# Kernel optimization log

Hardware: AMD Instinct MI355X
Metric: run time of the kernel (lower is better)

Reference implementation:

```python
import jax, jax.numpy as jnp
import numpy as np

B, D, E, K = 8192, 1024, 8, 2048  # tokens, dim, num_experts, k (per-expert capacity)


def setup_inputs() -> dict:
    key = jax.random.key(0)
    ks = jax.random.split(key, 5)
    x = jax.random.normal(ks[0], (B, D), dtype=jnp.float32)
    Wr = jax.random.normal(ks[1], (D, E), dtype=jnp.float32) * 0.02
    br = jnp.zeros((E,), jnp.float32)
    W1 = jax.random.normal(ks[2], (E, D, 4 * D), dtype=jnp.float32) * 0.02
    b1 = jnp.zeros((E, 4 * D), jnp.float32)
    W2 = jax.random.normal(ks[3], (E, 4 * D, D), dtype=jnp.float32) * 0.02
    b2 = jnp.zeros((E, D), jnp.float32)
    return {"x": x, "Wr": Wr, "br": br, "W1": W1, "b1": b1, "W2": W2, "b2": b2}


def _dispatch_weights(x, Wr, br):
    # Expert-choice routing: softmax over experts per token, each expert picks top-K tokens.
    gate = jax.nn.softmax(x @ Wr + br, axis=-1)          # [B, E]
    vals, idx = jax.lax.top_k(gate.T, K)                 # [E, K] each
    w = jnp.zeros((x.shape[0], E), x.dtype)
    w = w.at[idx.reshape(-1), jnp.repeat(jnp.arange(E), K)].set(vals.reshape(-1))
    # torch source builds dispatch_weights via .tolist(), detaching it from autograd
    return jax.lax.stop_gradient(w)                      # [B, E]


def reference(x, Wr, br, W1, b1, W2, b2):
    w = _dispatch_weights(x, Wr, br)                     # [B, E]
    mask = (w > 0).astype(x.dtype)                       # [B, E]
    xm = x[None, :, :] * mask.T[:, :, None]              # [E, B, D] (dense masked input, as in source)
    h = jax.nn.relu(jnp.einsum('ebd,edh->ebh', xm, W1) + b1[:, None, :])   # [E, B, 4D]
    y = jnp.einsum('ebh,ehd->ebd', h, W2) + b2[:, None, :]                 # [E, B, D]
    out = jnp.einsum('ebd,be->bd', y, w)                 # weighted combine over experts
    return out
```

## Files before the change

### kernel.cpp

```cpp
#include <hip/hip_runtime.h>
#include <hip/hip_bf16.h>

#define BTOK 8192
#define DDIM 1024
#define NEXP 8
#define KCAP 2048
#define HDIM 4096
#define MB ((size_t)1048576)

typedef __attribute__((ext_vector_type(4))) float f32x4;
typedef __attribute__((ext_vector_type(8))) short bf16x8;

__device__ __forceinline__ unsigned short f2bf(float f) {
    union { float f; unsigned u; } v; v.f = f;
    unsigned r = v.u + 0x7fffu + ((v.u >> 16) & 1u);
    return (unsigned short)(r >> 16);
}
__device__ __forceinline__ float bf2f(unsigned short u) {
    union { unsigned u; float f; } v; v.u = ((unsigned)u) << 16;
    return v.f;
}

typedef __attribute__((address_space(3))) unsigned int lds_u32;
typedef __attribute__((address_space(1))) const unsigned int glb_u32;
__device__ __forceinline__ void gl_lds16(const void* g, void* l) {
    __builtin_amdgcn_global_load_lds((glb_u32*)g, (lds_u32*)l, 16, 0, 0);
}

__global__ __launch_bounds__(256) void prep_kernel(
    const float* __restrict__ x, const float* __restrict__ Wr,
    const float* __restrict__ br, const float* __restrict__ W1,
    const float* __restrict__ W2, float* __restrict__ gateT,
    unsigned short* __restrict__ xb, unsigned short* __restrict__ w1t,
    unsigned short* __restrict__ w2t, int* __restrict__ inv) {
    __shared__ char smem[NEXP * DDIM * 4];
    int bid = blockIdx.x;
    int t = threadIdx.x;
    if (bid < BTOK / 4) {
        float (*wr_s)[DDIM] = (float (*)[DDIM])smem;
        for (int i = t; i < NEXP * DDIM; i += 256) {
            int e = i >> 10, d = i & 1023;
            wr_s[e][d] = Wr[d * NEXP + e];
        }
        if (t < 32) inv[(size_t)(t >> 2) * BTOK + bid * 4 + (t & 3)] = -1;
        __syncthreads();
        int wid = t >> 6, lane = t & 63;
        int b = bid * 4 + wid;
        const float4* xr = (const float4*)(x + (size_t)b * DDIM);
        float4 xv[4];
#pragma unroll
        for (int j = 0; j < 4; j++) xv[j] = xr[j * 64 + lane];
#pragma unroll
        for (int j = 0; j < 4; j++) {
            short4 s;
            s.x = (short)f2bf(xv[j].x); s.y = (short)f2bf(xv[j].y);
            s.z = (short)f2bf(xv[j].z); s.w = (short)f2bf(xv[j].w);
            *(short4*)(xb + (size_t)b * DDIM + (j * 64 + lane) * 4) = s;
        }
        double acc[NEXP];
#pragma unroll
        for (int e = 0; e < NEXP; e++) {
            double a = 0.0;
#pragma unroll
            for (int j = 0; j < 4; j++) {
                float4 wv = ((const float4*)&wr_s[e][0])[j * 64 + lane];
                a += (double)xv[j].x * wv.x + (double)xv[j].y * wv.y
                   + (double)xv[j].z * wv.z + (double)xv[j].w * wv.w;
            }
#pragma unroll
            for (int s = 1; s < 64; s <<= 1) a += __shfl_xor(a, s, 64);
            acc[e] = a + (double)br[e];
        }
        if (lane == 0) {
            double mx = acc[0];
#pragma unroll
            for (int e = 1; e < NEXP; e++) mx = fmax(mx, acc[e]);
            double p[NEXP]; double ssum = 0.0;
#pragma unroll
            for (int e = 0; e < NEXP; e++) { p[e] = exp(acc[e] - mx); ssum += p[e]; }
            double is = 1.0 / ssum;
#pragma unroll
            for (int e = 0; e < NEXP; e++) gateT[e * BTOK + b] = (float)(p[e] * is);
        }
    } else {
        int z16 = bid - BTOK / 4;
        int z = z16 >> 10, bx = z16 & 1023;
        const float* src; unsigned short* dst; int R, C;
        if (z < 8) { src = W1 + (size_t)z * DDIM * HDIM; dst = w1t + (size_t)z * DDIM * HDIM; R = DDIM; C = HDIM; }
        else       { src = W2 + (size_t)(z - 8) * DDIM * HDIM; dst = w2t + (size_t)(z - 8) * DDIM * HDIM; R = HDIM; C = DDIM; }
        int ntx = C >> 6;
        int c0 = (bx % ntx) * 64, r0 = (bx / ntx) * 64;
        unsigned short (*tile)[72] = (unsigned short (*)[72])smem;
        int cq = t & 15, rr = t >> 4;
#pragma unroll
        for (int ri = 0; ri < 4; ri++) {
            int r = ri * 16 + rr;
            float4 v = *(const float4*)(src + (size_t)(r0 + r) * C + c0 + cq * 4);
            tile[cq * 4 + 0][r] = f2bf(v.x);
            tile[cq * 4 + 1][r] = f2bf(v.y);
            tile[cq * 4 + 2][r] = f2bf(v.z);
            tile[cq * 4 + 3][r] = f2bf(v.w);
        }
        __syncthreads();
        int rq = t & 15, cc = t >> 4;
#pragma unroll
        for (int ci = 0; ci < 4; ci++) {
            int c = ci * 16 + cc;
            *(short4*)(dst + (size_t)(c0 + c) * R + r0 + rq * 4) = *(const short4*)&tile[c][rq * 4];
        }
    }
}

__global__ __launch_bounds__(256) void route_kernel(
    const float* __restrict__ gateT, int* __restrict__ idx_list,
    float* __restrict__ wt_list, int* __restrict__ inv) {
    int e = blockIdx.x, t = threadIdx.x;
    const float* g = gateT + (size_t)e * BTOK;
    __shared__ unsigned hist[256];
    __shared__ int pre[256];
    __shared__ unsigned sh_prefix;
    __shared__ int sh_rem;
    __shared__ unsigned cnt_s;
    if (t == 0) { sh_prefix = 0; sh_rem = KCAP; cnt_s = 0; }
    __syncthreads();
    for (int pass = 0; pass < 4; pass++) {
        int shift = 24 - pass * 8;
        hist[t] = 0;
        __syncthreads();
        unsigned pfx = sh_prefix;
        for (int i = t; i < BTOK; i += 256) {
            unsigned key = __float_as_uint(g[i]);
            if (pass == 0 || (key >> (shift + 8)) == pfx)
                atomicAdd(&hist[(key >> shift) & 255u], 1u);
        }
        __syncthreads();
        if (t == 0) {
            int rem = sh_rem, cum = 0, d = 0;
            for (int dd = 255; dd >= 0; dd--) {
                cum += (int)hist[dd];
                if (cum >= rem) { d = dd; break; }
            }
            sh_rem = rem - (cum - (int)hist[d]);
            sh_prefix = (pfx << 8) | (unsigned)d;
        }
        __syncthreads();
    }
    unsigned cutoff = sh_prefix;
    int base = t * 32;
    int ngt_t = 0, tie_t = 0;
    for (int j = 0; j < 32; j++) {
        unsigned key = __float_as_uint(g[base + j]);
        ngt_t += (key > cutoff) ? 1 : 0;
        tie_t += (key == cutoff) ? 1 : 0;
    }
    hist[t] = (unsigned)ngt_t;
    pre[t] = tie_t;
    __syncthreads();
    for (int s = 128; s > 0; s >>= 1) {
        if (t < s) hist[t] += hist[t + s];
        __syncthreads();
    }
    int need = KCAP - (int)hist[0];
    for (int s = 1; s < 256; s <<= 1) {
        int v = (t >= s) ? pre[t - s] : 0;
        __syncthreads();
        pre[t] += v;
        __syncthreads();
    }
    int rank = pre[t] - tie_t;
    for (int j = 0; j < 32; j++) {
        int b = base + j;
        float gv = g[b];
        unsigned key = __float_as_uint(gv);
        bool sel = (key > cutoff);
        if (!sel && key == cutoff) { sel = (rank < need); rank++; }
        if (sel) {
            unsigned pos = atomicAdd(&cnt_s, 1u);
            idx_list[(size_t)e * KCAP + pos] = b;
            wt_list[(size_t)e * KCAP + pos] = gv;
            inv[(size_t)e * BTOK + b] = (int)pos;
        }
    }
}


#define ASLOT 4096
#define BSLOT 8192
#define POOLB 49152
#define EPAD 136

__global__ __launch_bounds__(512, 4) void gemm1_kernel(
    const unsigned short* __restrict__ xb, const unsigned short* __restrict__ w1t,
    const float* __restrict__ b1, const int* __restrict__ idx_list,
    unsigned short* __restrict__ h) {
    extern __shared__ char pool[];
    unsigned short* As = (unsigned short*)pool;
    unsigned short* Bs = (unsigned short*)(pool + 2 * ASLOT * 2);
    int* toks = (int*)(pool + POOLB);
    int bid = blockIdx.x;
    int e = bid & 7, idx = bid >> 3;
    int m0 = (idx & 15) * 128, n0 = (idx >> 4) * 256;
    w1t      += (size_t)e * DDIM * HDIM;
    b1       += (size_t)e * HDIM;
    idx_list += (size_t)e * KCAP;
    h        += (size_t)e * KCAP * HDIM;
    int t = threadIdx.x;
    if (t < 128) toks[t] = idx_list[m0 + t];
    __syncthreads();
    int w = t >> 6, lane = t & 63, l4 = lane >> 2;
    unsigned swz = (unsigned)(((lane & 3) ^ ((lane >> 3) & 3)) << 4);
    const char* pa  = (const char*)(xb + (size_t)toks[w * 16 + l4] * DDIM) + swz;
    const char* pb0 = (const char*)(w1t + (size_t)(n0 + w * 16 + l4) * DDIM) + swz;
    const char* pb1 = (const char*)(w1t + (size_t)(n0 + 128 + w * 16 + l4) * DDIM) + swz;
    unsigned short* da  = As + (w * 16) * 32;
    unsigned short* db0 = Bs + (w * 16) * 32;
    unsigned short* db1 = Bs + (128 + w * 16) * 32;
#define ST1(slot, koff) do {                                         \
    gl_lds16(pa  + (koff), da  + (slot) * ASLOT);                    \
    gl_lds16(pb0 + (koff), db0 + (slot) * BSLOT);                    \
    gl_lds16(pb1 + (koff), db1 + (slot) * BSLOT); } while (0)
    int wm = w >> 2, wn = w & 3;
    int fr = lane & 15, kg = lane >> 4;
    unsigned koffr = (unsigned)((kg ^ ((fr >> 1) & 3)) << 4);
    const int NT = DDIM / 32;
    f32x4 acc[4][4] = {};
    ST1(0, 0);
    asm volatile("s_waitcnt vmcnt(0)" ::: "memory");
    __builtin_amdgcn_s_barrier();
    for (int kt = 0; kt < NT; kt++) {
        if (kt + 1 < NT) ST1((kt + 1) & 1, (size_t)(kt + 1) * 64);
        const char* ab = (const char*)As + (kt & 1) * (ASLOT * 2);
        const char* bb = (const char*)Bs + (kt & 1) * (BSLOT * 2);
        bf16x8 af[4], bf[4];
#pragma unroll
        for (int mf = 0; mf < 4; mf++)
            af[mf] = *(const bf16x8*)(ab + (wm * 64 + mf * 16 + fr) * 64 + koffr);
#pragma unroll
        for (int nf = 0; nf < 4; nf++)
            bf[nf] = *(const bf16x8*)(bb + (wn * 64 + nf * 16 + fr) * 64 + koffr);
        __builtin_amdgcn_s_setprio(1);
#pragma unroll
        for (int mf = 0; mf < 4; mf++)
#pragma unroll
            for (int nf = 0; nf < 4; nf++)
                acc[mf][nf] = __builtin_amdgcn_mfma_f32_16x16x32_bf16(
                    af[mf], bf[nf], acc[mf][nf], 0, 0, 0);
        __builtin_amdgcn_s_setprio(0);
        if (kt + 1 < NT) {
            asm volatile("s_waitcnt vmcnt(0)" ::: "memory");
            __builtin_amdgcn_s_barrier();
        }
    }
#undef ST1
    int hi = lane >> 4;
    float biasv[4];
#pragma unroll
    for (int nf = 0; nf < 4; nf++) biasv[nf] = b1[n0 + wn * 64 + nf * 16 + fr];
    unsigned short (*tile)[EPAD] = (unsigned short (*)[EPAD])pool;
#pragma unroll
    for (int p = 0; p < 2; p++) {
        __syncthreads();
        if ((wn >> 1) == p) {
            int lc = (wn & 1) * 64;
#pragma unroll
            for (int mf = 0; mf < 4; mf++)
#pragma unroll
                for (int nf = 0; nf < 4; nf++)
#pragma unroll
                    for (int r = 0; r < 4; r++)
                        tile[wm * 64 + mf * 16 + hi * 4 + r][lc + nf * 16 + fr] =
                            f2bf(fmaxf(acc[mf][nf][r] + biasv[nf], 0.f));
        }
        __syncthreads();
#pragma unroll
        for (int ps = 0; ps < 4; ps++) {
            int row = ps * 32 + (t >> 4);
            int c16 = t & 15;
            *(int4*)(h + (size_t)(m0 + row) * HDIM + n0 + p * 128 + c16 * 8) =
                *(const int4*)&tile[row][c16 * 8];
        }
    }
}

__global__ __launch_bounds__(512, 4) void gemm2y_kernel(
    const unsigned short* __restrict__ h, const unsigned short* __restrict__ w2t,
    const float* __restrict__ b2, const float* __restrict__ wt_list,
    unsigned short* __restrict__ yb) {
    __shared__ unsigned short As[2 * ASLOT];
    __shared__ unsigned short Bs[2 * BSLOT];
    __shared__ float wts[128];
    int bid = blockIdx.x;
    int e = bid & 7, idx = bid >> 3;
    int m0 = (idx & 15) * 128, n0 = (idx >> 4) * 256;
    h       += (size_t)e * KCAP * HDIM;
    w2t     += (size_t)e * DDIM * HDIM;
    b2      += (size_t)e * DDIM;
    wt_list += (size_t)e * KCAP;
    yb      += (size_t)e * KCAP * DDIM;
    int t = threadIdx.x;
    if (t < 128) wts[t] = wt_list[m0 + t];
    __syncthreads();
    int w = t >> 6, lane = t & 63, l4 = lane >> 2;
    unsigned swz = (unsigned)(((lane & 3) ^ ((lane >> 3) & 3)) << 4);
    const char* pa  = (const char*)(h + (size_t)(m0 + w * 16 + l4) * HDIM) + swz;
    const char* pb0 = (const char*)(w2t + (size_t)(n0 + w * 16 + l4) * HDIM) + swz;
    const char* pb1 = (const char*)(w2t + (size_t)(n0 + 128 + w * 16 + l4) * HDIM) + swz;
    unsigned short* da  = As + (w * 16) * 32;
    unsigned short* db0 = Bs + (w * 16) * 32;
    unsigned short* db1 = Bs + (128 + w * 16) * 32;
#define ST2(slot, koff) do {                                         \
    gl_lds16(pa  + (koff), da  + (slot) * ASLOT);                    \
    gl_lds16(pb0 + (koff), db0 + (slot) * BSLOT);                    \
    gl_lds16(pb1 + (koff), db1 + (slot) * BSLOT); } while (0)
    int wm = w >> 2, wn = w & 3;
    int fr = lane & 15, kg = lane >> 4;
    unsigned koffr = (unsigned)((kg ^ ((fr >> 1) & 3)) << 4);
    const int NT = HDIM / 32;
    f32x4 acc[4][4] = {};
    ST2(0, 0);
    asm volatile("s_waitcnt vmcnt(0)" ::: "memory");
    __builtin_amdgcn_s_barrier();
    for (int kt = 0; kt < NT; kt++) {
        if (kt + 1 < NT) ST2((kt + 1) & 1, (size_t)(kt + 1) * 64);
        const char* ab = (const char*)As + (kt & 1) * (ASLOT * 2);
        const char* bb = (const char*)Bs + (kt & 1) * (BSLOT * 2);
        bf16x8 af[4], bf[4];
#pragma unroll
        for (int mf = 0; mf < 4; mf++)
            af[mf] = *(const bf16x8*)(ab + (wm * 64 + mf * 16 + fr) * 64 + koffr);
#pragma unroll
        for (int nf = 0; nf < 4; nf++)
            bf[nf] = *(const bf16x8*)(bb + (wn * 64 + nf * 16 + fr) * 64 + koffr);
        __builtin_amdgcn_s_setprio(1);
#pragma unroll
        for (int mf = 0; mf < 4; mf++)
#pragma unroll
            for (int nf = 0; nf < 4; nf++)
                acc[mf][nf] = __builtin_amdgcn_mfma_f32_16x16x32_bf16(
                    af[mf], bf[nf], acc[mf][nf], 0, 0, 0);
        __builtin_amdgcn_s_setprio(0);
        if (kt + 1 < NT) {
            asm volatile("s_waitcnt vmcnt(0)" ::: "memory");
            __builtin_amdgcn_s_barrier();
        }
    }
#undef ST2
    int hi = lane >> 4;
#pragma unroll
    for (int nf = 0; nf < 4; nf++) {
        int col = n0 + wn * 64 + nf * 16 + fr;
        float bias = b2[col];
#pragma unroll
        for (int mf = 0; mf < 4; mf++) {
            int r0 = wm * 64 + mf * 16 + hi * 4;
#pragma unroll
            for (int r = 0; r < 4; r++) {
                int lrow = r0 + r;
                yb[(size_t)(m0 + lrow) * DDIM + col] = f2bf(wts[lrow] * (acc[mf][nf][r] + bias));
            }
        }
    }
}

__global__ __launch_bounds__(256) void combine_kernel(
    const unsigned short* __restrict__ yb, const int* __restrict__ inv,
    float* __restrict__ out) {
    int b = blockIdx.x, t = threadIdx.x;
    float4 acc = {0.f, 0.f, 0.f, 0.f};
#pragma unroll
    for (int e = 0; e < NEXP; e++) {
        int s = inv[(size_t)e * BTOK + b];
        if (s >= 0) {
            short4 v = *(const short4*)(yb + ((size_t)e * KCAP + s) * DDIM + t * 4);
            acc.x += bf2f((unsigned short)v.x);
            acc.y += bf2f((unsigned short)v.y);
            acc.z += bf2f((unsigned short)v.z);
            acc.w += bf2f((unsigned short)v.w);
        }
    }
    *(float4*)(out + (size_t)b * DDIM + t * 4) = acc;
}

extern "C" void kernel_launch(void* const* d_in, const int* in_sizes, int n_in,
                              void* d_out, int out_size, void* d_ws, size_t ws_size,
                              hipStream_t stream) {
    const float* x  = (const float*)d_in[0];
    const float* Wr = (const float*)d_in[1];
    const float* br = (const float*)d_in[2];
    const float* W1 = (const float*)d_in[3];
    const float* b1 = (const float*)d_in[4];
    const float* W2 = (const float*)d_in[5];
    const float* b2 = (const float*)d_in[6];
    float* out = (float*)d_out;

    char* ws = (char*)d_ws;
    float*    gateT    = (float*)ws;
    int*      idx_list = (int*)(ws + 327680);
    float*    wt_list  = (float*)(ws + 393216);
    int*      inv      = (int*)(ws + 458752);
    unsigned short* xbuf = (unsigned short*)(ws + 1 * MB);
    unsigned short* w1t  = (unsigned short*)(ws + 17 * MB);
    unsigned short* w2t  = (unsigned short*)(ws + 81 * MB);
    unsigned short* hbuf = (unsigned short*)(ws + 145 * MB);
    unsigned short* yb   = (unsigned short*)(ws + 273 * MB);
    const size_t NEED = 305 * MB;
    if (ws_size < NEED) return;

    prep_kernel<<<dim3(BTOK / 4 + 16384), 256, 0, stream>>>(
        x, Wr, br, W1, W2, gateT, xbuf, w1t, w2t, inv);
    route_kernel<<<dim3(NEXP), 256, 0, stream>>>(gateT, idx_list, wt_list, inv);

    gemm1_kernel<<<dim3((KCAP / 128) * (HDIM / 256) * NEXP), 512, POOLB + 512, stream>>>(
        xbuf, w1t, b1, idx_list, hbuf);
    gemm2y_kernel<<<dim3((KCAP / 128) * (DDIM / 256) * NEXP), 512, 0, stream>>>(
        hbuf, w2t, b2, wt_list, yb);
    combine_kernel<<<dim3(BTOK), 256, 0, stream>>>(yb, inv, out);
}
```

Before: 511.8 us.

## Fuse expert combine into GEMM2 epilogue via atomic scatter-add into output

Removes the bf16 per-expert y buffer, the inverse index map and the separate combine kernel. The GEMM2 epilogue now scatters weighted results directly into the fp32 output with atomicAdd, and the output is zeroed by a memset beforehand. This drops a 32MB intermediate write and read plus one launch. In exchange it issues many scalar fp32 atomics with a scattered access pattern, and the summation order across experts becomes nondeterministic.

```diff
diff --git a/kernel.cpp b/kernel.cpp
--- a/kernel.cpp
+++ b/kernel.cpp
@@ -16,10 +16,6 @@
     unsigned r = v.u + 0x7fffu + ((v.u >> 16) & 1u);
     return (unsigned short)(r >> 16);
 }
-__device__ __forceinline__ float bf2f(unsigned short u) {
-    union { unsigned u; float f; } v; v.u = ((unsigned)u) << 16;
-    return v.f;
-}
 
 typedef __attribute__((address_space(3))) unsigned int lds_u32;
 typedef __attribute__((address_space(1))) const unsigned int glb_u32;
@@ -32,7 +28,7 @@
     const float* __restrict__ br, const float* __restrict__ W1,
     const float* __restrict__ W2, float* __restrict__ gateT,
     unsigned short* __restrict__ xb, unsigned short* __restrict__ w1t,
-    unsigned short* __restrict__ w2t, int* __restrict__ inv) {
+    unsigned short* __restrict__ w2t) {
     __shared__ char smem[NEXP * DDIM * 4];
     int bid = blockIdx.x;
     int t = threadIdx.x;
@@ -42,7 +38,6 @@
             int e = i >> 10, d = i & 1023;
             wr_s[e][d] = Wr[d * NEXP + e];
         }
-        if (t < 32) inv[(size_t)(t >> 2) * BTOK + bid * 4 + (t & 3)] = -1;
         __syncthreads();
         int wid = t >> 6, lane = t & 63;
         int b = bid * 4 + wid;
@@ -113,7 +108,7 @@
 
 __global__ __launch_bounds__(256) void route_kernel(
     const float* __restrict__ gateT, int* __restrict__ idx_list,
-    float* __restrict__ wt_list, int* __restrict__ inv) {
+    float* __restrict__ wt_list) {
     int e = blockIdx.x, t = threadIdx.x;
     const float* g = gateT + (size_t)e * BTOK;
     __shared__ unsigned hist[256];
@@ -178,7 +173,6 @@
             unsigned pos = atomicAdd(&cnt_s, 1u);
             idx_list[(size_t)e * KCAP + pos] = b;
             wt_list[(size_t)e * KCAP + pos] = gv;
-            inv[(size_t)e * BTOK + b] = (int)pos;
         }
     }
 }
@@ -282,23 +276,24 @@
     }
 }
 
-__global__ __launch_bounds__(512, 4) void gemm2y_kernel(
+__global__ __launch_bounds__(512, 4) void gemm2o_kernel(
     const unsigned short* __restrict__ h, const unsigned short* __restrict__ w2t,
-    const float* __restrict__ b2, const float* __restrict__ wt_list,
-    unsigned short* __restrict__ yb) {
+    const float* __restrict__ b2, const int* __restrict__ idx_list,
+    const float* __restrict__ wt_list, float* __restrict__ out) {
     __shared__ unsigned short As[2 * ASLOT];
     __shared__ unsigned short Bs[2 * BSLOT];
     __shared__ float wts[128];
+    __shared__ int toks[128];
     int bid = blockIdx.x;
     int e = bid & 7, idx = bid >> 3;
     int m0 = (idx & 15) * 128, n0 = (idx >> 4) * 256;
-    h       += (size_t)e * KCAP * HDIM;
-    w2t     += (size_t)e * DDIM * HDIM;
-    b2      += (size_t)e * DDIM;
-    wt_list += (size_t)e * KCAP;
-    yb      += (size_t)e * KCAP * DDIM;
+    h        += (size_t)e * KCAP * HDIM;
+    w2t      += (size_t)e * DDIM * HDIM;
+    b2       += (size_t)e * DDIM;
+    wt_list  += (size_t)e * KCAP;
+    idx_list += (size_t)e * KCAP;
     int t = threadIdx.x;
-    if (t < 128) wts[t] = wt_list[m0 + t];
+    if (t < 128) { wts[t] = wt_list[m0 + t]; toks[t] = idx_list[m0 + t]; }
     __syncthreads();
     int w = t >> 6, lane = t & 63, l4 = lane >> 2;
     unsigned swz = (unsigned)(((lane & 3) ^ ((lane >> 3) & 3)) << 4);
@@ -356,29 +351,11 @@
 #pragma unroll
             for (int r = 0; r < 4; r++) {
                 int lrow = r0 + r;
-                yb[(size_t)(m0 + lrow) * DDIM + col] = f2bf(wts[lrow] * (acc[mf][nf][r] + bias));
+                atomicAdd(&out[(size_t)toks[lrow] * DDIM + col],
+                          wts[lrow] * (acc[mf][nf][r] + bias));
             }
         }
     }
-}
-
-__global__ __launch_bounds__(256) void combine_kernel(
-    const unsigned short* __restrict__ yb, const int* __restrict__ inv,
-    float* __restrict__ out) {
-    int b = blockIdx.x, t = threadIdx.x;
-    float4 acc = {0.f, 0.f, 0.f, 0.f};
-#pragma unroll
-    for (int e = 0; e < NEXP; e++) {
-        int s = inv[(size_t)e * BTOK + b];
-        if (s >= 0) {
-            short4 v = *(const short4*)(yb + ((size_t)e * KCAP + s) * DDIM + t * 4);
-            acc.x += bf2f((unsigned short)v.x);
-            acc.y += bf2f((unsigned short)v.y);
-            acc.z += bf2f((unsigned short)v.z);
-            acc.w += bf2f((unsigned short)v.w);
-        }
-    }
-    *(float4*)(out + (size_t)b * DDIM + t * 4) = acc;
 }
 
 extern "C" void kernel_launch(void* const* d_in, const int* in_sizes, int n_in,
@@ -397,22 +374,21 @@
     float*    gateT    = (float*)ws;
     int*      idx_list = (int*)(ws + 327680);
     float*    wt_list  = (float*)(ws + 393216);
-    int*      inv      = (int*)(ws + 458752);
     unsigned short* xbuf = (unsigned short*)(ws + 1 * MB);
     unsigned short* w1t  = (unsigned short*)(ws + 17 * MB);
     unsigned short* w2t  = (unsigned short*)(ws + 81 * MB);
     unsigned short* hbuf = (unsigned short*)(ws + 145 * MB);
-    unsigned short* yb   = (unsigned short*)(ws + 273 * MB);
-    const size_t NEED = 305 * MB;
+    const size_t NEED = 273 * MB;
     if (ws_size < NEED) return;
 
+    hipMemsetAsync(out, 0, (size_t)out_size * sizeof(float), stream);
+
     prep_kernel<<<dim3(BTOK / 4 + 16384), 256, 0, stream>>>(
-        x, Wr, br, W1, W2, gateT, xbuf, w1t, w2t, inv);
-    route_kernel<<<dim3(NEXP), 256, 0, stream>>>(gateT, idx_list, wt_list, inv);
+        x, Wr, br, W1, W2, gateT, xbuf, w1t, w2t);
+    route_kernel<<<dim3(NEXP), 256, 0, stream>>>(gateT, idx_list, wt_list);
 
     gemm1_kernel<<<dim3((KCAP / 128) * (HDIM / 256) * NEXP), 512, POOLB + 512, stream>>>(
         xbuf, w1t, b1, idx_list, hbuf);
-    gemm2y_kernel<<<dim3((KCAP / 128) * (DDIM / 256) * NEXP), 512, 0, stream>>>(
-        hbuf, w2t, b2, wt_list, yb);
-    combine_kernel<<<dim3(BTOK), 256, 0, stream>>>(yb, inv, out);
-}
+    gemm2o_kernel<<<dim3((KCAP / 128) * (DDIM / 256) * NEXP), 512, 0, stream>>>(
+        hbuf, w2t, b2, idx_list, wt_list, out);
+}
```

New measurement: 533.3 us. 1.04x slower.
